# Optimization experiments

Measured on AMD Instinct MI355X. Metric: run time of the kernel, lower is better.

Reference implementation:

```python
import jax, jax.numpy as jnp
import numpy as np

B, S, D = 2, 2048, 4096
NH, NKV = 32, 8
HD = D // NH  # 128
N_REP = NH // NKV  # 4


def setup_inputs() -> dict:
    key = jax.random.key(0)
    ks = jax.random.split(key, 5)
    scale = 0.02
    return {
        "x": jax.random.normal(ks[0], (B, S, D), dtype=jnp.float32),
        "wq": jax.random.normal(ks[1], (D, NH * HD), dtype=jnp.float32) * scale,
        "wk": jax.random.normal(ks[2], (D, NKV * HD), dtype=jnp.float32) * scale,
        "wv": jax.random.normal(ks[3], (D, NKV * HD), dtype=jnp.float32) * scale,
        "wo": jax.random.normal(ks[4], (NH * HD, D), dtype=jnp.float32) * scale,
    }


def reference(x, wq, wk, wv, wo):
    bsz, toks, _ = x.shape
    q = (x @ wq).reshape(bsz, toks, NH, HD)      # [B,S,NH,HD]
    k = (x @ wk).reshape(bsz, toks, NKV, HD)     # [B,S,NKV,HD]
    v = (x @ wv).reshape(bsz, toks, NKV, HD)
    # GQA: fold n_rep into einsum instead of materializing repeated K/V.
    qg = q.reshape(bsz, toks, NKV, N_REP, HD)    # group query heads per kv head
    scores = jnp.einsum('bqgrd,bkgd->bgrqk', qg, k) / jnp.sqrt(jnp.asarray(HD, x.dtype))
    attn = jax.nn.softmax(scores.astype(jnp.float32), axis=-1).astype(x.dtype)
    out = jnp.einsum('bgrqk,bkgd->bqgrd', attn, v)  # [B,S,NKV,N_REP,HD]
    out = out.reshape(bsz, toks, NH * HD)
    return out @ wo
```

## Files before the change

kernel.cpp:

```cpp
#include <hip/hip_runtime.h>
#include <math.h>

typedef _Float16 f16;
using f16x8 = __attribute__((ext_vector_type(8))) _Float16;
using f32x4 = __attribute__((ext_vector_type(4))) float;

#define BATCH 2
#define SEQ   2048
#define DMODEL 4096
#define NH    32
#define NKV   8
#define HD    128
#define MTOK  (BATCH*SEQ)

__global__ __launch_bounds__(256) void cvt_f32_f16_k(const float* __restrict__ in,
                                                     f16* __restrict__ out, int n8) {
  int i = blockIdx.x * 256 + threadIdx.x;
  if (i >= n8) return;
  const float4* p = reinterpret_cast<const float4*>(in) + (size_t)i * 2;
  float4 a = p[0], b = p[1];
  f16x8 o = { (f16)a.x, (f16)a.y, (f16)a.z, (f16)a.w,
              (f16)b.x, (f16)b.y, (f16)b.z, (f16)b.w };
  reinterpret_cast<f16x8*>(out)[i] = o;
}

__global__ __launch_bounds__(256) void transpose_cvt_k(const float* __restrict__ w,
                                                       f16* __restrict__ wt, int Kd, int Nd) {
  __shared__ float tile[32][33];
  const int t = threadIdx.x;
  const int n0 = blockIdx.x * 32, k0 = blockIdx.y * 32;
  const int r = t >> 3, c4 = (t & 7) << 2;
  const float4 v = *reinterpret_cast<const float4*>(w + (size_t)(k0 + r) * Nd + n0 + c4);
  tile[r][c4 + 0] = v.x; tile[r][c4 + 1] = v.y; tile[r][c4 + 2] = v.z; tile[r][c4 + 3] = v.w;
  __syncthreads();
  union { f16 h[4]; ushort4 u4; } pk;
  pk.h[0] = (f16)tile[c4 + 0][r];
  pk.h[1] = (f16)tile[c4 + 1][r];
  pk.h[2] = (f16)tile[c4 + 2][r];
  pk.h[3] = (f16)tile[c4 + 3][r];
  *reinterpret_cast<ushort4*>(wt + (size_t)(n0 + r) * Kd + k0 + c4) = pk.u4;
}

template<int MODE>
__global__ __launch_bounds__(256) void gemm_bt_k(const f16* __restrict__ A,
                                                 const f16* __restrict__ BT,
                                                 void* __restrict__ Cv,
                                                 int M, int N, int K) {
  __shared__ f16 Alds[128 * 64];
  __shared__ f16 Blds[128 * 64];
  const int t = threadIdx.x, lane = t & 63, w = t >> 6;
  const int nbn = N >> 7;
  const int nwg = gridDim.x;
  const int cpx = nwg >> 3;
  const int bid = blockIdx.x;
  const int swz = (bid & 7) * cpx + (bid >> 3);
  const int bm = swz / nbn, bn = swz % nbn;
  const size_t m0 = (size_t)bm << 7, n0 = (size_t)bn << 7;

  const int srow = t >> 3;
  const int sslot = t & 7;
  char* ldsAw = (char*)Alds + w * 1024;
  char* ldsBw = (char*)Blds + w * 1024;

  f32x4 acc[4][4];
#pragma unroll
  for (int i = 0; i < 4; i++)
#pragma unroll
    for (int j = 0; j < 4; j++) acc[i][j] = f32x4{0.f, 0.f, 0.f, 0.f};

  const int wr = (w >> 1) << 6, wc = (w & 1) << 6;
  const int ll = lane & 15, lg = lane >> 4;

  for (int kt = 0; kt < K; kt += 64) {
    __syncthreads();
#pragma unroll
    for (int p = 0; p < 4; p++) {
      const int row = srow + (p << 5);
      const int ssrc = (sslot ^ (row & 7)) << 3;
      const f16* gA = A + (m0 + row) * (size_t)K + kt + ssrc;
      __builtin_amdgcn_global_load_lds((const __attribute__((address_space(1))) void*)gA,
          (__attribute__((address_space(3))) void*)(ldsAw + p * 4096), 16, 0, 0);
      const f16* gB = BT + (n0 + row) * (size_t)K + kt + ssrc;
      __builtin_amdgcn_global_load_lds((const __attribute__((address_space(1))) void*)gB,
          (__attribute__((address_space(3))) void*)(ldsBw + p * 4096), 16, 0, 0);
    }
    __syncthreads();
#pragma unroll
    for (int kk = 0; kk < 2; kk++) {
      f16x8 af[4], bfr[4];
      const int slot = (kk << 2) + lg;
#pragma unroll
      for (int i = 0; i < 4; i++) {
        const int r = wr + (i << 4) + ll;
        af[i] = *reinterpret_cast<const f16x8*>((const char*)Alds + r * 128 + ((slot ^ (r & 7)) << 4));
      }
#pragma unroll
      for (int j = 0; j < 4; j++) {
        const int r = wc + (j << 4) + ll;
        bfr[j] = *reinterpret_cast<const f16x8*>((const char*)Blds + r * 128 + ((slot ^ (r & 7)) << 4));
      }
#pragma unroll
      for (int i = 0; i < 4; i++)
#pragma unroll
        for (int j = 0; j < 4; j++)
          acc[i][j] = __builtin_amdgcn_mfma_f32_16x16x32_f16(af[i], bfr[j], acc[i][j], 0, 0, 0);
    }
  }

#pragma unroll
  for (int i = 0; i < 4; i++) {
    const size_t mrow = m0 + wr + (i << 4) + (lg << 2);
#pragma unroll
    for (int j = 0; j < 4; j++) {
      const size_t ncol = n0 + wc + (j << 4) + ll;
      if (MODE == 0) {
        f16* C = (f16*)Cv;
#pragma unroll
        for (int r = 0; r < 4; r++) C[(mrow + r) * N + ncol] = (f16)acc[i][j][r];
      } else if (MODE == 1) {
        f16* C = (f16*)Cv;
        const int kvh = (int)(ncol >> 7), d = (int)(ncol & 127);
        const int b = (int)(mrow >> 11), s = (int)(mrow & 2047);
        union { f16 h[4]; ushort4 u4; } pk;
#pragma unroll
        for (int r = 0; r < 4; r++) pk.h[r] = (f16)acc[i][j][r];
        *reinterpret_cast<ushort4*>(C + (((size_t)(b * NKV + kvh) * HD + d) * SEQ + s)) = pk.u4;
      } else {
        float* C = (float*)Cv;
#pragma unroll
        for (int r = 0; r < 4; r++) C[(mrow + r) * N + ncol] = acc[i][j][r];
      }
    }
  }
}

template<int MODE>
__global__ __launch_bounds__(512, 2) void gemm256_k(const f16* __restrict__ A,
                                                    const f16* __restrict__ BT,
                                                    void* __restrict__ Cv,
                                                    int M, int N, int K) {
  __shared__ f16 lds[2 * 4 * 128 * 64];
  char* ldsb = (char*)lds;

  const int t = threadIdx.x, lane = t & 63, w = t >> 6;
  const int wm = w >> 2, wn = w & 3;
  const int ll = lane & 15, lg = lane >> 4;
  const int nbn = N >> 8;
  const int nwg = gridDim.x, cpx = nwg >> 3, bid = blockIdx.x;
  const int swz = (bid & 7) * cpx + (bid >> 3);
  const int bm = swz / nbn, bn = swz % nbn;
  const size_t m0 = (size_t)bm << 8, n0 = (size_t)bn << 8;
  const int NT = K >> 6;

  auto stage = [&](int bufI, int unit, int ktS) {
    const f16* base = (unit < 2) ? (A + (m0 + (size_t)(unit & 1) * 128) * (size_t)K)
                                 : (BT + (n0 + (size_t)(unit & 1) * 128) * (size_t)K);
#pragma unroll
    for (int rr = 0; rr < 2; rr++) {
      const int u = t + rr * 512;
      const int row = u >> 3, lin = u & 7;
      const int slot = lin ^ (row & 7);
      const f16* src = base + (size_t)row * K + ktS + slot * 8;
      char* dst = ldsb + (size_t)(bufI * 4 + unit) * 16384 + (size_t)(w * 64 + rr * 512) * 16;
      __builtin_amdgcn_global_load_lds((const __attribute__((address_space(1))) void*)src,
          (__attribute__((address_space(3))) void*)dst, 16, 0, 0);
    }
  };

  f32x4 acc[8][4];
#pragma unroll
  for (int i = 0; i < 8; i++)
#pragma unroll
    for (int j = 0; j < 4; j++) acc[i][j] = f32x4{0.f, 0.f, 0.f, 0.f};

  f16x8 af[4][2];
  f16x8 bfr[2][2][2];

  stage(0, 0, 0); stage(0, 2, 0); stage(0, 3, 0); stage(0, 1, 0);
  stage(1, 0, 64); stage(1, 2, 64); stage(1, 3, 64);
  asm volatile("s_waitcnt vmcnt(6)" ::: "memory");
  __builtin_amdgcn_sched_barrier(0);
  __builtin_amdgcn_s_barrier();

#define PH(RBUF, RDA, RDB, SBUF, SUNIT, STILE, VM, MH, NHQ) do {                          \
    if ((RDA) >= 0) {                                                                     \
      const char* ab = ldsb + (size_t)((RBUF) * 4 + (RDA)) * 16384;                       \
      _Pragma("unroll") for (int mi = 0; mi < 4; mi++)                                    \
        _Pragma("unroll") for (int kk = 0; kk < 2; kk++)                                  \
          af[mi][kk] = *reinterpret_cast<const f16x8*>(ab + (mi * 32 + wm * 16 + ll) * 128\
                               + ((((kk << 2) + lg) ^ (ll & 7)) << 4));                   \
    }                                                                                     \
    if ((RDB) >= 0) {                                                                     \
      const char* bb = ldsb + (size_t)((RBUF) * 4 + 2 + (RDB)) * 16384;                   \
      _Pragma("unroll") for (int ni = 0; ni < 2; ni++)                                    \
        _Pragma("unroll") for (int kk = 0; kk < 2; kk++)                                  \
          bfr[RDB][ni][kk] = *reinterpret_cast<const f16x8*>(bb +                         \
                               (wn * 32 + ni * 16 + ll) * 128                             \
                               + ((((kk << 2) + lg) ^ (ll & 7)) << 4));                   \
    }                                                                                     \
    stage((SBUF), (SUNIT), ((STILE) & (NT - 1)) << 6);                                    \
    if (VM) { asm volatile("s_waitcnt vmcnt(6)" ::: "memory");                            \
              __builtin_amdgcn_sched_barrier(0); }                                        \
    __builtin_amdgcn_s_barrier();                                                         \
    asm volatile("s_waitcnt lgkmcnt(0)" ::: "memory");                                    \
    __builtin_amdgcn_sched_barrier(0);                                                    \
    __builtin_amdgcn_s_setprio(1);                                                        \
    _Pragma("unroll") for (int kk = 0; kk < 2; kk++)                                      \
      _Pragma("unroll") for (int mi = 0; mi < 4; mi++)                                    \
        _Pragma("unroll") for (int ni = 0; ni < 2; ni++)                                  \
          acc[(MH) * 4 + mi][(NHQ) * 2 + ni] = __builtin_amdgcn_mfma_f32_16x16x32_f16(    \
              af[mi][kk], bfr[NHQ][ni][kk], acc[(MH) * 4 + mi][(NHQ) * 2 + ni], 0, 0, 0); \
    __builtin_amdgcn_s_setprio(0);                                                        \
    __builtin_amdgcn_s_barrier();                                                         \
  } while (0)

  for (int tt = 0; tt < NT; tt += 2) {
    PH(0,  0,  0, 1, 1, tt + 1, false, 0, 0);
    PH(0, -1,  1, 0, 0, tt + 2, false, 0, 1);
    PH(0,  1, -1, 0, 2, tt + 2, false, 1, 0);
    PH(0, -1, -1, 0, 3, tt + 2, true , 1, 1);
    PH(1,  0,  0, 0, 1, tt + 2, false, 0, 0);
    PH(1, -1,  1, 1, 0, tt + 3, false, 0, 1);
    PH(1,  1, -1, 1, 2, tt + 3, false, 1, 0);
    PH(1, -1, -1, 1, 3, tt + 3, true , 1, 1);
  }
#undef PH

#pragma unroll
  for (int mh = 0; mh < 2; mh++)
#pragma unroll
    for (int mi = 0; mi < 4; mi++) {
      const size_t r0 = m0 + mh * 128 + mi * 32 + wm * 16 + lg * 4;
#pragma unroll
      for (int nh = 0; nh < 2; nh++)
#pragma unroll
        for (int ni = 0; ni < 2; ni++) {
          const size_t c = n0 + nh * 128 + wn * 32 + ni * 16 + ll;
          const f32x4 v = acc[mh * 4 + mi][nh * 2 + ni];
          if (MODE == 0) {
            f16* C = (f16*)Cv;
#pragma unroll
            for (int rr = 0; rr < 4; rr++) C[(r0 + rr) * N + c] = (f16)v[rr];
          } else {
            float* C = (float*)Cv;
#pragma unroll
            for (int rr = 0; rr < 4; rr++) C[(r0 + rr) * N + c] = v[rr];
          }
        }
    }
}

__global__ __launch_bounds__(512) void attn_k4(const f16* __restrict__ Q,
                                               const f16* __restrict__ Kb,
                                               const f16* __restrict__ VT,
                                               f16* __restrict__ ctx) {
  __shared__ f16 Klds[2][64 * 128];
  __shared__ f16 Vlds[2][128 * 64];
  __shared__ f16 Plds[8][16 * 64];

  const int t = threadIdx.x, lane = t & 63, w = t >> 6;
  const int bid = blockIdx.x;
  const int swz = (bid & 7) * 128 + (bid >> 3);
  const int qt = swz & 63, kvh = (swz >> 6) & 7, b = swz >> 9;
  const int h = kvh * 4 + (w & 3);
  const int q0 = qt * 32 + (w >> 2) * 16;
  const int ll = lane & 15, lg = lane >> 4;

  const f16* Qb = Q + ((size_t)(b * SEQ + q0) * NH + h) * HD;
  const f16* Kh = Kb + ((size_t)b * SEQ * NKV + kvh) * HD;
  const f16* Vh = VT + ((size_t)(b * NKV + kvh)) * HD * SEQ;

  const float KSC2 = 0.08838834764831845f * 1.4426950408889634f;
  f16x8 qf[4];
#pragma unroll
  for (int kd = 0; kd < 4; kd++) {
    qf[kd] = *reinterpret_cast<const f16x8*>(Qb + (size_t)ll * (NH * HD) + kd * 32 + lg * 8);
#pragma unroll
    for (int j = 0; j < 8; j++) qf[kd][j] = (f16)((float)qf[kd][j] * KSC2);
  }

  float m_ = -INFINITY;
  float l_ = 0.f;
  f32x4 o[8];
#pragma unroll
  for (int df = 0; df < 8; df++) o[df] = f32x4{0.f, 0.f, 0.f, 0.f};

  const float THR = 11.5416f;

  auto stage = [&](int bufi, int kt) {
#pragma unroll
    for (int rr = 0; rr < 2; rr++) {
      const int u = w * 128 + rr * 64 + lane;
      const int krow = u >> 4, klin = u & 15;
      const int kslot = klin ^ (krow & 7);
      const f16* ksrc = Kh + (size_t)(kt + krow) * (NKV * HD) + kslot * 8;
      __builtin_amdgcn_global_load_lds((const __attribute__((address_space(1))) void*)ksrc,
          (__attribute__((address_space(3))) void*)((char*)&Klds[bufi][0] + (size_t)(w * 128 + rr * 64) * 16),
          16, 0, 0);
      const int vrow = u >> 3, vlin = u & 7;
      const int vslot = vlin ^ (vrow & 7);
      const f16* vsrc = Vh + (size_t)vrow * SEQ + kt + vslot * 8;
      __builtin_amdgcn_global_load_lds((const __attribute__((address_space(1))) void*)vsrc,
          (__attribute__((address_space(3))) void*)((char*)&Vlds[bufi][0] + (size_t)(w * 128 + rr * 64) * 16),
          16, 0, 0);
    }
  };

  stage(0, 0);
  __syncthreads();

  for (int kt = 0; kt < SEQ; kt += 64) {
    const int buf = (kt >> 6) & 1;
    if (kt + 64 < SEQ) stage(buf ^ 1, kt + 64);

    const char* Kt = (const char*)Klds[buf];
    const char* Vt = (const char*)Vlds[buf];

    f32x4 s[4];
#pragma unroll
    for (int nf = 0; nf < 4; nf++) {
      f32x4 a = f32x4{0.f, 0.f, 0.f, 0.f};
#pragma unroll
      for (int kd = 0; kd < 4; kd++) {
        const int row = nf * 16 + ll;
        f16x8 kf = *reinterpret_cast<const f16x8*>(
            Kt + row * 256 + ((((kd << 2) + lg) ^ (row & 7)) << 4));
        a = __builtin_amdgcn_mfma_f32_16x16x32_f16(kf, qf[kd], a, 0, 0, 0);
      }
      s[nf] = a;
    }

    float mx = s[0][0];
#pragma unroll
    for (int nf = 0; nf < 4; nf++)
#pragma unroll
      for (int r = 0; r < 4; r++) mx = fmaxf(mx, s[nf][r]);

    if (!__all((int)(mx <= m_ + THR))) {
      float mr = fmaxf(mx, __shfl_xor(mx, 16, 64));
      mr = fmaxf(mr, __shfl_xor(mr, 32, 64));
      const float mn = fmaxf(m_, mr);
      const float corrq = __builtin_amdgcn_exp2f(m_ - mn);
      m_ = mn;
      l_ *= corrq;
#pragma unroll
      for (int r = 0; r < 4; r++) {
        const float c = __shfl(corrq, (lane & 48) | (lg * 4 + r), 64);
#pragma unroll
        for (int df = 0; df < 8; df++) o[df][r] *= c;
      }
    }

    float rs = 0.f;
#pragma unroll
    for (int nf = 0; nf < 4; nf++)
#pragma unroll
      for (int r = 0; r < 4; r++) {
        const float p = __builtin_amdgcn_exp2f(s[nf][r] - m_);
        s[nf][r] = p;
        rs += p;
      }
    rs += __shfl_xor(rs, 16, 64);
    rs += __shfl_xor(rs, 32, 64);
    l_ += rs;

    char* Pw = (char*)&Plds[w][0];
#pragma unroll
    for (int nf = 0; nf < 4; nf++) {
      union { f16 h[4]; ushort4 u4; } pk;
#pragma unroll
      for (int r = 0; r < 4; r++) pk.h[r] = (f16)s[nf][r];
      *reinterpret_cast<ushort4*>(Pw + ll * 128 + ((nf * 32 + lg * 8) ^ ((ll & 7) << 4))) = pk.u4;
    }

    f16x8 pf[2];
#pragma unroll
    for (int kf = 0; kf < 2; kf++)
      pf[kf] = *reinterpret_cast<const f16x8*>(Pw + ll * 128 + (((kf << 6) + (lg << 4)) ^ ((ll & 7) << 4)));

#pragma unroll
    for (int kf = 0; kf < 2; kf++)
#pragma unroll
      for (int df = 0; df < 8; df++) {
        const int row = df * 16 + ll;
        f16x8 vf = *reinterpret_cast<const f16x8*>(
            Vt + row * 128 + ((((kf << 2) + lg) ^ (row & 7)) << 4));
        o[df] = __builtin_amdgcn_mfma_f32_16x16x32_f16(pf[kf], vf, o[df], 0, 0, 0);
      }

    __syncthreads();
  }

  float inv[4];
#pragma unroll
  for (int r = 0; r < 4; r++) {
    const float lq = __shfl(l_, (lane & 48) | (lg * 4 + r), 64);
    inv[r] = 1.0f / lq;
  }
  f16* cb = ctx + ((size_t)(b * SEQ + q0) * NH + h) * HD;
#pragma unroll
  for (int df = 0; df < 8; df++)
#pragma unroll
    for (int r = 0; r < 4; r++)
      cb[(size_t)(lg * 4 + r) * (NH * HD) + df * 16 + ll] = (f16)(o[df][r] * inv[r]);
}

extern "C" void kernel_launch(void* const* d_in, const int* in_sizes, int n_in,
                              void* d_out, int out_size, void* d_ws, size_t ws_size,
                              hipStream_t stream) {
  (void)in_sizes; (void)n_in; (void)out_size;
  const float* x  = (const float*)d_in[0];
  const float* wq = (const float*)d_in[1];
  const float* wk = (const float*)d_in[2];
  const float* wv = (const float*)d_in[3];
  const float* wo = (const float*)d_in[4];
  float* out = (float*)d_out;

  const size_t SZ_X  = (size_t)MTOK * DMODEL * sizeof(f16);
  const size_t SZ_KV = (size_t)MTOK * NKV * HD * sizeof(f16);
  if (ws_size < 3 * SZ_X + 2 * SZ_KV) return;

  char* ws = (char*)d_ws;
  f16* xh  = (f16*)ws;
  f16* wT  = (f16*)(ws + SZ_X);
  f16* Qb  = (f16*)(ws + 2 * SZ_X);
  f16* Kb  = (f16*)(ws + 3 * SZ_X);
  f16* VTb = (f16*)(ws + 3 * SZ_X + SZ_KV);

  cvt_f32_f16_k<<<dim3(MTOK * DMODEL / 8 / 256), 256, 0, stream>>>(x, xh, MTOK * DMODEL / 8);

  transpose_cvt_k<<<dim3(DMODEL / 32, DMODEL / 32), 256, 0, stream>>>(wq, wT, DMODEL, DMODEL);
  gemm256_k<0><<<dim3((MTOK / 256) * (DMODEL / 256)), 512, 0, stream>>>(xh, wT, Qb, MTOK, DMODEL, DMODEL);

  transpose_cvt_k<<<dim3(NKV * HD / 32, DMODEL / 32), 256, 0, stream>>>(wk, wT, DMODEL, NKV * HD);
  gemm_bt_k<0><<<dim3((MTOK / 128) * ((NKV * HD) / 128)), 256, 0, stream>>>(xh, wT, Kb, MTOK, NKV * HD, DMODEL);

  transpose_cvt_k<<<dim3(NKV * HD / 32, DMODEL / 32), 256, 0, stream>>>(wv, wT, DMODEL, NKV * HD);
  gemm_bt_k<1><<<dim3((MTOK / 128) * ((NKV * HD) / 128)), 256, 0, stream>>>(xh, wT, VTb, MTOK, NKV * HD, DMODEL);

  attn_k4<<<dim3(BATCH * NKV * (SEQ / 32)), 512, 0, stream>>>(Qb, Kb, VTb, xh);

  transpose_cvt_k<<<dim3(DMODEL / 32, DMODEL / 32), 256, 0, stream>>>(wo, wT, DMODEL, DMODEL);
  gemm256_k<2><<<dim3((MTOK / 256) * (DMODEL / 256)), 512, 0, stream>>>(xh, wT, out, MTOK, DMODEL, DMODEL);
}
```

Before: 615.3 us.

## Fuse K/V projections into one GEMM and software-pipeline attention QK with PV

The K and V projection GEMMs are merged into a single launch over a concatenated transposed weight (N=2048). A new epilogue mode writes the first half row-major as K and the second half transposed as V. The attention kernel is restructured so each iteration computes QK scores for the current tile while running softmax and PV for the previous tile. It uses explicit vmcnt waits and raw barriers instead of __syncthreads, and raises occupancy hints via launch_bounds(512,4). The aim is to hide MFMA/exp latency and remove a launch, at the cost of extra live registers for the carried score tile and fragile hand-managed synchronisation.

```diff
diff --git a/kernel.cpp b/kernel.cpp
--- a/kernel.cpp
+++ b/kernel.cpp
@@ -117,18 +117,25 @@
         f16* C = (f16*)Cv;
 #pragma unroll
         for (int r = 0; r < 4; r++) C[(mrow + r) * N + ncol] = (f16)acc[i][j][r];
-      } else if (MODE == 1) {
-        f16* C = (f16*)Cv;
-        const int kvh = (int)(ncol >> 7), d = (int)(ncol & 127);
-        const int b = (int)(mrow >> 11), s = (int)(mrow & 2047);
-        union { f16 h[4]; ushort4 u4; } pk;
-#pragma unroll
-        for (int r = 0; r < 4; r++) pk.h[r] = (f16)acc[i][j][r];
-        *reinterpret_cast<ushort4*>(C + (((size_t)(b * NKV + kvh) * HD + d) * SEQ + s)) = pk.u4;
-      } else {
+      } else if (MODE == 2) {
         float* C = (float*)Cv;
 #pragma unroll
         for (int r = 0; r < 4; r++) C[(mrow + r) * N + ncol] = acc[i][j][r];
+      } else if (MODE == 3) {
+        f16* Kc = (f16*)Cv;
+        f16* Vt = (f16*)Cv + (size_t)MTOK * NKV * HD;
+        if ((int)ncol < 1024) {
+#pragma unroll
+          for (int r = 0; r < 4; r++) Kc[(mrow + r) * 1024 + ncol] = (f16)acc[i][j][r];
+        } else {
+          const int nc = (int)ncol - 1024;
+          const int kvh = nc >> 7, d = nc & 127;
+          const int b = (int)(mrow >> 11), sc = (int)(mrow & 2047);
+          union { f16 h[4]; ushort4 u4; } pk;
+#pragma unroll
+          for (int r = 0; r < 4; r++) pk.h[r] = (f16)acc[i][j][r];
+          *reinterpret_cast<ushort4*>(Vt + (((size_t)(b * NKV + kvh) * HD + d) * SEQ + sc)) = pk.u4;
+        }
       }
     }
   }
@@ -250,10 +257,10 @@
     }
 }
 
-__global__ __launch_bounds__(512) void attn_k4(const f16* __restrict__ Q,
-                                               const f16* __restrict__ Kb,
-                                               const f16* __restrict__ VT,
-                                               f16* __restrict__ ctx) {
+__global__ __launch_bounds__(512, 4) void attn_k5(const f16* __restrict__ Q,
+                                                  const f16* __restrict__ Kb,
+                                                  const f16* __restrict__ VT,
+                                                  f16* __restrict__ ctx) {
   __shared__ f16 Klds[2][64 * 128];
   __shared__ f16 Vlds[2][128 * 64];
   __shared__ f16 Plds[8][16 * 64];
@@ -284,10 +291,11 @@
   f32x4 o[8];
 #pragma unroll
   for (int df = 0; df < 8; df++) o[df] = f32x4{0.f, 0.f, 0.f, 0.f};
+  f32x4 sP[4];
 
   const float THR = 11.5416f;
 
-  auto stage = [&](int bufi, int kt) {
+  auto stageK = [&](int bufi, int kt) {
 #pragma unroll
     for (int rr = 0; rr < 2; rr++) {
       const int u = w * 128 + rr * 64 + lane;
@@ -295,46 +303,27 @@
       const int kslot = klin ^ (krow & 7);
       const f16* ksrc = Kh + (size_t)(kt + krow) * (NKV * HD) + kslot * 8;
       __builtin_amdgcn_global_load_lds((const __attribute__((address_space(1))) void*)ksrc,
-          (__attribute__((address_space(3))) void*)((char*)&Klds[bufi][0] + (size_t)(w * 128 + rr * 64) * 16),
-          16, 0, 0);
+          (__attribute__((address_space(3))) void*)((char*)&Klds[bufi][0] + (size_t)u * 16), 16, 0, 0);
+    }
+  };
+  auto stageV = [&](int bufi, int kt) {
+#pragma unroll
+    for (int rr = 0; rr < 2; rr++) {
+      const int u = w * 128 + rr * 64 + lane;
       const int vrow = u >> 3, vlin = u & 7;
       const int vslot = vlin ^ (vrow & 7);
       const f16* vsrc = Vh + (size_t)vrow * SEQ + kt + vslot * 8;
       __builtin_amdgcn_global_load_lds((const __attribute__((address_space(1))) void*)vsrc,
-          (__attribute__((address_space(3))) void*)((char*)&Vlds[bufi][0] + (size_t)(w * 128 + rr * 64) * 16),
-          16, 0, 0);
+          (__attribute__((address_space(3))) void*)((char*)&Vlds[bufi][0] + (size_t)u * 16), 16, 0, 0);
     }
   };
 
-  stage(0, 0);
-  __syncthreads();
-
-  for (int kt = 0; kt < SEQ; kt += 64) {
-    const int buf = (kt >> 6) & 1;
-    if (kt + 64 < SEQ) stage(buf ^ 1, kt + 64);
-
-    const char* Kt = (const char*)Klds[buf];
-    const char* Vt = (const char*)Vlds[buf];
-
-    f32x4 s[4];
-#pragma unroll
-    for (int nf = 0; nf < 4; nf++) {
-      f32x4 a = f32x4{0.f, 0.f, 0.f, 0.f};
-#pragma unroll
-      for (int kd = 0; kd < 4; kd++) {
-        const int row = nf * 16 + ll;
-        f16x8 kf = *reinterpret_cast<const f16x8*>(
-            Kt + row * 256 + ((((kd << 2) + lg) ^ (row & 7)) << 4));
-        a = __builtin_amdgcn_mfma_f32_16x16x32_f16(kf, qf[kd], a, 0, 0, 0);
-      }
-      s[nf] = a;
-    }
-
-    float mx = s[0][0];
+  auto processPrev = [&](const char* Vt) {
+    float mx = sP[0][0];
 #pragma unroll
     for (int nf = 0; nf < 4; nf++)
 #pragma unroll
-      for (int r = 0; r < 4; r++) mx = fmaxf(mx, s[nf][r]);
+      for (int r = 0; r < 4; r++) mx = fmaxf(mx, sP[nf][r]);
 
     if (!__all((int)(mx <= m_ + THR))) {
       float mr = fmaxf(mx, __shfl_xor(mx, 16, 64));
@@ -356,8 +345,8 @@
     for (int nf = 0; nf < 4; nf++)
 #pragma unroll
       for (int r = 0; r < 4; r++) {
-        const float p = __builtin_amdgcn_exp2f(s[nf][r] - m_);
-        s[nf][r] = p;
+        const float p = __builtin_amdgcn_exp2f(sP[nf][r] - m_);
+        sP[nf][r] = p;
         rs += p;
       }
     rs += __shfl_xor(rs, 16, 64);
@@ -369,7 +358,7 @@
     for (int nf = 0; nf < 4; nf++) {
       union { f16 h[4]; ushort4 u4; } pk;
 #pragma unroll
-      for (int r = 0; r < 4; r++) pk.h[r] = (f16)s[nf][r];
+      for (int r = 0; r < 4; r++) pk.h[r] = (f16)sP[nf][r];
       *reinterpret_cast<ushort4*>(Pw + ll * 128 + ((nf * 32 + lg * 8) ^ ((ll & 7) << 4))) = pk.u4;
     }
 
@@ -387,9 +376,47 @@
             Vt + row * 128 + ((((kf << 2) + lg) ^ (row & 7)) << 4));
         o[df] = __builtin_amdgcn_mfma_f32_16x16x32_f16(pf[kf], vf, o[df], 0, 0, 0);
       }
-
-    __syncthreads();
-  }
+  };
+
+  stageK(0, 0);
+  stageV(0, 0);
+
+  const int NT = SEQ / 64;
+  for (int i = 0; i < NT; i++) {
+    asm volatile("s_waitcnt vmcnt(2)" ::: "memory");
+    __builtin_amdgcn_sched_barrier(0);
+    __builtin_amdgcn_s_barrier();
+
+    const char* Kt = (const char*)Klds[i & 1];
+    f32x4 sN[4];
+#pragma unroll
+    for (int nf = 0; nf < 4; nf++) {
+      f32x4 a = f32x4{0.f, 0.f, 0.f, 0.f};
+#pragma unroll
+      for (int kd = 0; kd < 4; kd++) {
+        const int row = nf * 16 + ll;
+        f16x8 kf = *reinterpret_cast<const f16x8*>(
+            Kt + row * 256 + ((((kd << 2) + lg) ^ (row & 7)) << 4));
+        a = __builtin_amdgcn_mfma_f32_16x16x32_f16(kf, qf[kd], a, 0, 0, 0);
+      }
+      sN[nf] = a;
+    }
+
+    if (i > 0) processPrev((const char*)Vlds[(i - 1) & 1]);
+
+    __builtin_amdgcn_s_barrier();
+    if (i + 1 < NT) {
+      stageK((i + 1) & 1, (i + 1) * 64);
+      stageV((i + 1) & 1, (i + 1) * 64);
+    }
+#pragma unroll
+    for (int nf = 0; nf < 4; nf++) sP[nf] = sN[nf];
+  }
+
+  asm volatile("s_waitcnt vmcnt(0)" ::: "memory");
+  __builtin_amdgcn_sched_barrier(0);
+  __builtin_amdgcn_s_barrier();
+  processPrev((const char*)Vlds[(NT - 1) & 1]);
 
   float inv[4];
 #pragma unroll
@@ -433,12 +460,10 @@
   gemm256_k<0><<<dim3((MTOK / 256) * (DMODEL / 256)), 512, 0, stream>>>(xh, wT, Qb, MTOK, DMODEL, DMODEL);
 
   transpose_cvt_k<<<dim3(NKV * HD / 32, DMODEL / 32), 256, 0, stream>>>(wk, wT, DMODEL, NKV * HD);
-  gemm_bt_k<0><<<dim3((MTOK / 128) * ((NKV * HD) / 128)), 256, 0, stream>>>(xh, wT, Kb, MTOK, NKV * HD, DMODEL);
-
-  transpose_cvt_k<<<dim3(NKV * HD / 32, DMODEL / 32), 256, 0, stream>>>(wv, wT, DMODEL, NKV * HD);
-  gemm_bt_k<1><<<dim3((MTOK / 128) * ((NKV * HD) / 128)), 256, 0, stream>>>(xh, wT, VTb, MTOK, NKV * HD, DMODEL);
-
-  attn_k4<<<dim3(BATCH * NKV * (SEQ / 32)), 512, 0, stream>>>(Qb, Kb, VTb, xh);
+  transpose_cvt_k<<<dim3(NKV * HD / 32, DMODEL / 32), 256, 0, stream>>>(wv, wT + (size_t)1024 * DMODEL, DMODEL, NKV * HD);
+  gemm_bt_k<3><<<dim3((MTOK / 128) * (2048 / 128)), 256, 0, stream>>>(xh, wT, Kb, MTOK, 2048, DMODEL);
+
+  attn_k5<<<dim3(BATCH * NKV * (SEQ / 32)), 512, 0, stream>>>(Qb, Kb, VTb, xh);
 
   transpose_cvt_k<<<dim3(DMODEL / 32, DMODEL / 32), 256, 0, stream>>>(wo, wT, DMODEL, DMODEL);
   gemm256_k<2><<<dim3((MTOK / 256) * (DMODEL / 256)), 512, 0, stream>>>(xh, wT, out, MTOK, DMODEL, DMODEL);
```

After: 642.8 us. 4.5% more time.

## Fuse K and V projections into one GEMM and fold softmax scale into Wq

Applied to the files above, without the earlier changes.

Concatenates the transposed K and V weights into one 2048-column matrix so a single GEMM computes both projections, writing K row-major and V transposed from the epilogue. It also pre-multiplies Wq by the softmax scale times log2(e) during conversion, which removes the per-thread Q rescaling in the attention kernel. This saves one launch and one pass over x, and gives the fused GEMM a larger grid. The cost is a branchy epilogue and a slight change in fp16 rounding of Q.

```diff
diff --git a/kernel.cpp b/kernel.cpp
--- a/kernel.cpp
+++ b/kernel.cpp
@@ -25,7 +25,8 @@
 }
 
 __global__ __launch_bounds__(256) void transpose_cvt_k(const float* __restrict__ w,
-                                                       f16* __restrict__ wt, int Kd, int Nd) {
+                                                       f16* __restrict__ wt, int Kd, int Nd,
+                                                       float scale) {
   __shared__ float tile[32][33];
   const int t = threadIdx.x;
   const int n0 = blockIdx.x * 32, k0 = blockIdx.y * 32;
@@ -34,10 +35,10 @@
   tile[r][c4 + 0] = v.x; tile[r][c4 + 1] = v.y; tile[r][c4 + 2] = v.z; tile[r][c4 + 3] = v.w;
   __syncthreads();
   union { f16 h[4]; ushort4 u4; } pk;
-  pk.h[0] = (f16)tile[c4 + 0][r];
-  pk.h[1] = (f16)tile[c4 + 1][r];
-  pk.h[2] = (f16)tile[c4 + 2][r];
-  pk.h[3] = (f16)tile[c4 + 3][r];
+  pk.h[0] = (f16)(tile[c4 + 0][r] * scale);
+  pk.h[1] = (f16)(tile[c4 + 1][r] * scale);
+  pk.h[2] = (f16)(tile[c4 + 2][r] * scale);
+  pk.h[3] = (f16)(tile[c4 + 3][r] * scale);
   *reinterpret_cast<ushort4*>(wt + (size_t)(n0 + r) * Kd + k0 + c4) = pk.u4;
 }
 
@@ -117,18 +118,25 @@
         f16* C = (f16*)Cv;
 #pragma unroll
         for (int r = 0; r < 4; r++) C[(mrow + r) * N + ncol] = (f16)acc[i][j][r];
-      } else if (MODE == 1) {
-        f16* C = (f16*)Cv;
-        const int kvh = (int)(ncol >> 7), d = (int)(ncol & 127);
-        const int b = (int)(mrow >> 11), s = (int)(mrow & 2047);
-        union { f16 h[4]; ushort4 u4; } pk;
-#pragma unroll
-        for (int r = 0; r < 4; r++) pk.h[r] = (f16)acc[i][j][r];
-        *reinterpret_cast<ushort4*>(C + (((size_t)(b * NKV + kvh) * HD + d) * SEQ + s)) = pk.u4;
-      } else {
+      } else if (MODE == 2) {
         float* C = (float*)Cv;
 #pragma unroll
         for (int r = 0; r < 4; r++) C[(mrow + r) * N + ncol] = acc[i][j][r];
+      } else if (MODE == 3) {
+        f16* Kc = (f16*)Cv;
+        f16* Vt = (f16*)Cv + (size_t)MTOK * NKV * HD;
+        if ((int)ncol < 1024) {
+#pragma unroll
+          for (int r = 0; r < 4; r++) Kc[(mrow + r) * 1024 + ncol] = (f16)acc[i][j][r];
+        } else {
+          const int nc = (int)ncol - 1024;
+          const int kvh = nc >> 7, d = nc & 127;
+          const int b = (int)(mrow >> 11), sc = (int)(mrow & 2047);
+          union { f16 h[4]; ushort4 u4; } pk;
+#pragma unroll
+          for (int r = 0; r < 4; r++) pk.h[r] = (f16)acc[i][j][r];
+          *reinterpret_cast<ushort4*>(Vt + (((size_t)(b * NKV + kvh) * HD + d) * SEQ + sc)) = pk.u4;
+        }
       }
     }
   }
@@ -250,7 +258,7 @@
     }
 }
 
-__global__ __launch_bounds__(512) void attn_k4(const f16* __restrict__ Q,
+__global__ __launch_bounds__(512) void attn_k7(const f16* __restrict__ Q,
                                                const f16* __restrict__ Kb,
                                                const f16* __restrict__ VT,
                                                f16* __restrict__ ctx) {
@@ -270,14 +278,10 @@
   const f16* Kh = Kb + ((size_t)b * SEQ * NKV + kvh) * HD;
   const f16* Vh = VT + ((size_t)(b * NKV + kvh)) * HD * SEQ;
 
-  const float KSC2 = 0.08838834764831845f * 1.4426950408889634f;
   f16x8 qf[4];
 #pragma unroll
-  for (int kd = 0; kd < 4; kd++) {
+  for (int kd = 0; kd < 4; kd++)
     qf[kd] = *reinterpret_cast<const f16x8*>(Qb + (size_t)ll * (NH * HD) + kd * 32 + lg * 8);
-#pragma unroll
-    for (int j = 0; j < 8; j++) qf[kd][j] = (f16)((float)qf[kd][j] * KSC2);
-  }
 
   float m_ = -INFINITY;
   float l_ = 0.f;
@@ -295,14 +299,12 @@
       const int kslot = klin ^ (krow & 7);
       const f16* ksrc = Kh + (size_t)(kt + krow) * (NKV * HD) + kslot * 8;
       __builtin_amdgcn_global_load_lds((const __attribute__((address_space(1))) void*)ksrc,
-          (__attribute__((address_space(3))) void*)((char*)&Klds[bufi][0] + (size_t)(w * 128 + rr * 64) * 16),
-          16, 0, 0);
+          (__attribute__((address_space(3))) void*)((char*)&Klds[bufi][0] + (size_t)u * 16), 16, 0, 0);
       const int vrow = u >> 3, vlin = u & 7;
       const int vslot = vlin ^ (vrow & 7);
       const f16* vsrc = Vh + (size_t)vrow * SEQ + kt + vslot * 8;
       __builtin_amdgcn_global_load_lds((const __attribute__((address_space(1))) void*)vsrc,
-          (__attribute__((address_space(3))) void*)((char*)&Vlds[bufi][0] + (size_t)(w * 128 + rr * 64) * 16),
-          16, 0, 0);
+          (__attribute__((address_space(3))) void*)((char*)&Vlds[bufi][0] + (size_t)u * 16), 16, 0, 0);
     }
   };
 
@@ -427,19 +429,19 @@
   f16* Kb  = (f16*)(ws + 3 * SZ_X);
   f16* VTb = (f16*)(ws + 3 * SZ_X + SZ_KV);
 
+  const float KSC2 = 0.08838834764831845f * 1.4426950408889634f;
+
   cvt_f32_f16_k<<<dim3(MTOK * DMODEL / 8 / 256), 256, 0, stream>>>(x, xh, MTOK * DMODEL / 8);
 
-  transpose_cvt_k<<<dim3(DMODEL / 32, DMODEL / 32), 256, 0, stream>>>(wq, wT, DMODEL, DMODEL);
+  transpose_cvt_k<<<dim3(DMODEL / 32, DMODEL / 32), 256, 0, stream>>>(wq, wT, DMODEL, DMODEL, KSC2);
   gemm256_k<0><<<dim3((MTOK / 256) * (DMODEL / 256)), 512, 0, stream>>>(xh, wT, Qb, MTOK, DMODEL, DMODEL);
 
-  transpose_cvt_k<<<dim3(NKV * HD / 32, DMODEL / 32), 256, 0, stream>>>(wk, wT, DMODEL, NKV * HD);
-  gemm_bt_k<0><<<dim3((MTOK / 128) * ((NKV * HD) / 128)), 256, 0, stream>>>(xh, wT, Kb, MTOK, NKV * HD, DMODEL);
-
-  transpose_cvt_k<<<dim3(NKV * HD / 32, DMODEL / 32), 256, 0, stream>>>(wv, wT, DMODEL, NKV * HD);
-  gemm_bt_k<1><<<dim3((MTOK / 128) * ((NKV * HD) / 128)), 256, 0, stream>>>(xh, wT, VTb, MTOK, NKV * HD, DMODEL);
-
-  attn_k4<<<dim3(BATCH * NKV * (SEQ / 32)), 512, 0, stream>>>(Qb, Kb, VTb, xh);
-
-  transpose_cvt_k<<<dim3(DMODEL / 32, DMODEL / 32), 256, 0, stream>>>(wo, wT, DMODEL, DMODEL);
+  transpose_cvt_k<<<dim3(NKV * HD / 32, DMODEL / 32), 256, 0, stream>>>(wk, wT, DMODEL, NKV * HD, 1.0f);
+  transpose_cvt_k<<<dim3(NKV * HD / 32, DMODEL / 32), 256, 0, stream>>>(wv, wT + (size_t)1024 * DMODEL, DMODEL, NKV * HD, 1.0f);
+  gemm_bt_k<3><<<dim3((MTOK / 128) * (2048 / 128)), 256, 0, stream>>>(xh, wT, Kb, MTOK, 2048, DMODEL);
+
+  attn_k7<<<dim3(BATCH * NKV * (SEQ / 32)), 512, 0, stream>>>(Qb, Kb, VTb, xh);
+
+  transpose_cvt_k<<<dim3(DMODEL / 32, DMODEL / 32), 256, 0, stream>>>(wo, wT, DMODEL, DMODEL, 1.0f);
   gemm256_k<2><<<dim3((MTOK / 256) * (DMODEL / 256)), 512, 0, stream>>>(xh, wT, out, MTOK, DMODEL, DMODEL);
 }
```

Result: faster. 551.4 us (-10.4%).
